# Kernel optimization log

Hardware: AMD Instinct MI355X
Metric: run time of the kernel (lower is better)

Reference implementation:

```python
import jax, jax.numpy as jnp
import numpy as np

EPS = 1e-5  # torch LayerNorm default
H, DH = 8, 64  # heads, dim_head


def _ln(x, g, b):
    mu = jnp.mean(x, axis=-1, keepdims=True)
    var = jnp.var(x, axis=-1, keepdims=True)
    return (x - mu) / jnp.sqrt(var + EPS) * g + b


def setup_inputs() -> dict:
    key = jax.random.key(0)
    ks = jax.random.split(key, 8)
    B, N, M, D, CD = 4, 2048, 256, 1024, 768
    J = M + 1 + N  # context + null + self
    return {
        "x": jax.random.normal(ks[0], (B, N, D), jnp.float32),
        "context": jax.random.normal(ks[1], (B, M, CD), jnp.float32),
        "att_bias": jax.random.normal(ks[2], (B, H, N, J), jnp.float32) * 0.02,
        "ln_g": jnp.ones((D,), jnp.float32),
        "ln_b": jnp.zeros((D,), jnp.float32),
        "null_kv": jax.random.normal(ks[3], (2, DH), jnp.float32),
        "Wq": jax.random.normal(ks[4], (D, H * DH), jnp.float32) * 0.02,
        "Wkv": jax.random.normal(ks[5], (D, 2 * DH), jnp.float32) * 0.02,
        "cln_g": jnp.ones((CD,), jnp.float32),
        "cln_b": jnp.zeros((CD,), jnp.float32),
        "Wc": jax.random.normal(ks[6], (CD, 2 * DH), jnp.float32) * 0.02,
        "bc": jnp.zeros((2 * DH,), jnp.float32),
        "Wo": jax.random.normal(ks[7], (H * DH, D), jnp.float32) * 0.02,
        "oln_g": jnp.ones((D,), jnp.float32),
        "oln_b": jnp.zeros((D,), jnp.float32),
    }


def reference(x, context, att_bias, ln_g, ln_b, null_kv, Wq, Wkv,
              cln_g, cln_b, Wc, bc, Wo, oln_g, oln_b):
    B, N, D = x.shape
    scale = DH ** -0.5
    xn = _ln(x, ln_g, ln_b)
    # queries: per-head [b,h,n,dh], pre-scaled
    q = (xn @ Wq).reshape(B, N, H, DH).transpose(0, 2, 1, 3) * scale
    # shared single-head k/v [b,n,dh]
    kv = xn @ Wkv
    k, v = kv[..., :DH], kv[..., DH:]
    # context k/v [b,m,dh]
    ckv = _ln(context, cln_g, cln_b) @ Wc + bc
    ck, cv = ckv[..., :DH], ckv[..., DH:]
    # null kv token [b,1,dh]
    nk = jnp.broadcast_to(null_kv[0], (B, 1, DH))
    nv = jnp.broadcast_to(null_kv[1], (B, 1, DH))
    # torch order: cat null first, then context -> (ck, nk, k)
    k = jnp.concatenate([ck, nk, k], axis=1)  # [b, j, dh]
    v = jnp.concatenate([cv, nv, v], axis=1)
    score = jnp.einsum('bhid,bjd->bhij', q, k) + att_bias
    probs = jax.nn.softmax(score.astype(jnp.float32), axis=-1).astype(v.dtype)
    att = jnp.einsum('bhij,bjd->bhid', probs, v)
    att = att.transpose(0, 2, 1, 3).reshape(B, N, H * DH)
    return _ln(att @ Wo, oln_g, oln_b)
```

## Files before the change

kernel.cpp:

```cpp
#include <hip/hip_runtime.h>
#include <hip/hip_bf16.h>
#include <cstdint>
#include <cstddef>

#define Bq  4
#define Nq  2048
#define Mq  256
#define Dq  1024
#define CDq 768
#define Hq  8
#define DHq 64
#define Jq  2305
#define QKVN 640
#define NCH 37
#define J2  (NCH * 64)

typedef __bf16  bf16x8 __attribute__((ext_vector_type(8)));
typedef float   f32x4  __attribute__((ext_vector_type(4)));
typedef float   f32x4u __attribute__((ext_vector_type(4), aligned(4)));
typedef float   f32x16 __attribute__((ext_vector_type(16)));
typedef short   s16x8  __attribute__((ext_vector_type(8)));
typedef short   s16x4  __attribute__((ext_vector_type(4)));
typedef unsigned int u32x4 __attribute__((ext_vector_type(4)));
typedef unsigned short u16;
typedef unsigned int   u32;

__device__ __forceinline__ u16 f2b(float v) {
  unsigned x = __builtin_bit_cast(unsigned, v);
  unsigned r = (x + 0x7fffu + ((x >> 16) & 1u)) >> 16;
  return (u16)r;
}
__device__ __forceinline__ float b2f(u16 u) {
  unsigned x = ((unsigned)u) << 16;
  return __builtin_bit_cast(float, x);
}
__device__ __forceinline__ u32 cvtpk(float lo, float hi) {
  u32 r;
  asm("v_cvt_pk_bf16_f32 %0, %1, %2" : "=v"(r) : "v"(lo), "v"(hi));
  return r;
}
__device__ __forceinline__ void pswap(u32& a, u32& b) {
  asm volatile("v_permlane32_swap_b32 %0, %1" : "+v"(a), "+v"(b));
}
__device__ __forceinline__ f32x4 mfma16(bf16x8 a, bf16x8 b, f32x4 c) {
  return __builtin_amdgcn_mfma_f32_16x16x32_bf16(a, b, c, 0, 0, 0);
}
__device__ __forceinline__ f32x16 mfma32(bf16x8 a, bf16x8 b, f32x16 c) {
  return __builtin_amdgcn_mfma_f32_32x32x16_bf16(a, b, c, 0, 0, 0);
}
__device__ __forceinline__ bf16x8 frag_ld(const u16* p) {
  return __builtin_bit_cast(bf16x8, *(const s16x8*)p);
}
__device__ __forceinline__ void stout(float* p, float v) { *p = v; }
__device__ __forceinline__ void stout(u16*   p, float v) { *p = f2b(v); }

__device__ __forceinline__ void gl_lds16(const void* gSrc, void* ldsDst) {
  __builtin_amdgcn_global_load_lds(
      (const __attribute__((address_space(1))) void*)gSrc,
      (__attribute__((address_space(3))) void*)ldsDst, 16, 0, 0);
}

__global__ __launch_bounds__(256) void prep_kernel(
    const float* __restrict__ x,   const float* __restrict__ ln_g,
    const float* __restrict__ ln_b, u16* __restrict__ xn,
    const float* __restrict__ ctx, const float* __restrict__ cln_g,
    const float* __restrict__ cln_b, u16* __restrict__ ctxn,
    const float* __restrict__ Wq, const float* __restrict__ Wkv,
    const float* __restrict__ Wc, const float* __restrict__ Wo,
    u16* __restrict__ WqkvT, u16* __restrict__ WcT, u16* __restrict__ WoT) {
  const int tid = threadIdx.x;
  if (blockIdx.x < Bq * Nq + Bq * Mq) {
    const int row = blockIdx.x;
    const float* in; const float* g; const float* bb; u16* out; int D;
    if (row < Bq * Nq) {
      in = x + (size_t)row * Dq; g = ln_g; bb = ln_b;
      out = xn + (size_t)row * Dq; D = Dq;
    } else {
      int r2 = row - Bq * Nq;
      in = ctx + (size_t)r2 * CDq; g = cln_g; bb = cln_b;
      out = ctxn + (size_t)r2 * CDq; D = CDq;
    }
    __shared__ float buf[1024];
    __shared__ float red[8];
    float s = 0.f, s2 = 0.f;
    for (int i = tid; i < D; i += 256) {
      float v = in[i];
      buf[i] = v;
      s += v; s2 += v * v;
    }
    #pragma unroll
    for (int off = 32; off; off >>= 1) {
      s  += __shfl_down(s,  off);
      s2 += __shfl_down(s2, off);
    }
    if ((tid & 63) == 0) { red[tid >> 6] = s; red[4 + (tid >> 6)] = s2; }
    __syncthreads();
    float sum = red[0] + red[1] + red[2] + red[3];
    float sq  = red[4] + red[5] + red[6] + red[7];
    float mean = sum / D;
    float var  = sq / D - mean * mean;
    float rstd = rsqrtf(var + 1e-5f);
    for (int i = tid; i < D; i += 256)
      out[i] = f2b((buf[i] - mean) * rstd * g[i] + bb[i]);
  } else {
    __shared__ float T[32][33];
    int bid = blockIdx.x - (Bq * Nq + Bq * Mq);
    const float* W; u16* WT; int K, N, bx, by;
    if (bid < 512)      { W = Wq;  WT = WqkvT;                    K = 1024; N = 512;  bx = bid % 16;        by = bid / 16; }
    else if (bid < 640) { W = Wkv; WT = WqkvT + (size_t)512*1024; K = 1024; N = 128;  bx = (bid-512) % 4;   by = (bid-512) / 4; }
    else if (bid < 736) { W = Wc;  WT = WcT;                      K = 768;  N = 128;  bx = (bid-640) % 4;   by = (bid-640) / 4; }
    else                { W = Wo;  WT = WoT;                      K = 512;  N = 1024; bx = (bid-736) % 32;  by = (bid-736) / 32; }
    const int n0 = bx * 32, k0 = by * 32;
    const int tx = tid & 31, ty = tid >> 5;
    #pragma unroll
    for (int i = 0; i < 32; i += 8)
      T[ty + i][tx] = W[(size_t)(k0 + ty + i) * N + n0 + tx];
    __syncthreads();
    #pragma unroll
    for (int i = 0; i < 32; i += 8)
      WT[(size_t)(n0 + ty + i) * K + k0 + tx] = f2b(T[tx][ty + i]);
  }
}

__global__ __launch_bounds__(256) void ln_out_kernel(
    const u16* __restrict__ in, const float* __restrict__ g,
    const float* __restrict__ bb, float* __restrict__ out) {
  const int row = blockIdx.x;
  const int tid = threadIdx.x;
  __shared__ float buf[1024];
  __shared__ float red[8];
  const u16* xr = in + (size_t)row * Dq;
  float s = 0.f, s2 = 0.f;
  {
    s16x4 v4 = *(const s16x4*)(xr + tid * 4);
    #pragma unroll
    for (int e = 0; e < 4; ++e) {
      float v = b2f((u16)v4[e]);
      buf[tid * 4 + e] = v;
      s += v; s2 += v * v;
    }
  }
  #pragma unroll
  for (int off = 32; off; off >>= 1) {
    s  += __shfl_down(s,  off);
    s2 += __shfl_down(s2, off);
  }
  if ((tid & 63) == 0) { red[tid >> 6] = s; red[4 + (tid >> 6)] = s2; }
  __syncthreads();
  float sum = red[0] + red[1] + red[2] + red[3];
  float sq  = red[4] + red[5] + red[6] + red[7];
  float mean = sum / Dq;
  float var  = sq / Dq - mean * mean;
  float rstd = rsqrtf(var + 1e-5f);
  #pragma unroll
  for (int e = 0; e < 4; ++e) {
    int i = tid * 4 + e;
    out[(size_t)row * Dq + i] = (buf[i] - mean) * rstd * g[i] + bb[i];
  }
}

template <typename OT>
__device__ __forceinline__ void gemm_body(const u16* __restrict__ A,
                                          const u16* __restrict__ BT,
                                          OT* __restrict__ C,
                                          int N, int K, int m0, int n0,
                                          u16* Al, u16* Bl) {
  const int tid  = threadIdx.x;
  const int lane = tid & 63, wave = tid >> 6;
  const int l16  = lane & 15, lhi = lane >> 4;
  const int wm = (wave >> 1) * 64, wn = (wave & 1) * 64;

  const int offB = (wave << 10) + (lane << 4);
  const int srow = offB >> 6;
  const int scby = offB & 63;

  f32x4 acc[4][4];
  #pragma unroll
  for (int i = 0; i < 4; ++i)
    #pragma unroll
    for (int j = 0; j < 4; ++j) acc[i][j] = f32x4{0.f, 0.f, 0.f, 0.f};

  for (int k0 = 0; k0 < K; k0 += 32) {
    __syncthreads();
    #pragma unroll
    for (int c = 0; c < 2; ++c) {
      gl_lds16((const char*)(A  + (size_t)(m0 + srow + c * 64) * K + k0) + scby,
               (char*)Al + c * 4096 + (wave << 10));
      gl_lds16((const char*)(BT + (size_t)(n0 + srow + c * 64) * K + k0) + scby,
               (char*)Bl + c * 4096 + (wave << 10));
    }
    __syncthreads();

    bf16x8 af[4], bfr[4];
    #pragma unroll
    for (int mt = 0; mt < 4; ++mt)
      af[mt] = frag_ld(Al + (wm + mt * 16 + l16) * 32 + lhi * 8);
    #pragma unroll
    for (int nt = 0; nt < 4; ++nt)
      bfr[nt] = frag_ld(Bl + (wn + nt * 16 + l16) * 32 + lhi * 8);
    __builtin_amdgcn_s_setprio(1);
    #pragma unroll
    for (int mt = 0; mt < 4; ++mt)
      #pragma unroll
      for (int nt = 0; nt < 4; ++nt)
        acc[mt][nt] = mfma16(af[mt], bfr[nt], acc[mt][nt]);
    __builtin_amdgcn_s_setprio(0);
  }

  #pragma unroll
  for (int mt = 0; mt < 4; ++mt)
    #pragma unroll
    for (int nt = 0; nt < 4; ++nt)
      #pragma unroll
      for (int r = 0; r < 4; ++r)
        stout(C + (size_t)(m0 + wm + mt * 16 + lhi * 4 + r) * N
                + (n0 + wn + nt * 16 + l16),
              acc[mt][nt][r]);
}

__global__ __launch_bounds__(256) void gemm_qkv_ckv(
    const u16* __restrict__ xn, const u16* __restrict__ WqkvT,
    u16* __restrict__ qkv,
    const u16* __restrict__ ctxn, const u16* __restrict__ WcT,
    u16* __restrict__ ckvb) {
  const u16 *A, *BT; u16* C; int N, K, m0, n0;
  if (blockIdx.y < 5) {
    A = xn; BT = WqkvT; C = qkv; N = QKVN; K = Dq;
    m0 = blockIdx.x * 128; n0 = blockIdx.y * 128;
  } else {
    if (blockIdx.x >= 8) return;
    A = ctxn; BT = WcT; C = ckvb; N = 2 * DHq; K = CDq;
    m0 = blockIdx.x * 128; n0 = 0;
  }
  __shared__ __align__(16) u16 Al[128 * 32];
  __shared__ __align__(16) u16 Bl[128 * 32];
  gemm_body<u16>(A, BT, C, N, K, m0, n0, Al, Bl);
}

__global__ __launch_bounds__(256) void gemm128b(const u16* __restrict__ A,
                                                const u16* __restrict__ BT,
                                                u16* __restrict__ C,
                                                int N, int K) {
  __shared__ __align__(16) u16 Al[128 * 32];
  __shared__ __align__(16) u16 Bl[128 * 32];
  gemm_body<u16>(A, BT, C, N, K, blockIdx.x * 128, blockIdx.y * 128, Al, Bl);
}

__global__ void build_kv(const u16* __restrict__ qkv,
                         const u16* __restrict__ ckvb,
                         const float* __restrict__ nullkv,
                         const float* __restrict__ bc,
                         u16* __restrict__ Kt, u16* __restrict__ Vt) {
  int idx = blockIdx.x * 256 + threadIdx.x;
  if (idx >= Bq * J2 * 64) return;
  int d = idx & 63;
  int t = idx >> 6;
  int j = t % J2;
  int b = t / J2;
  float k = 0.f, v = 0.f;
  if (j < Mq) {
    const u16* p = ckvb + (size_t)(b * Mq + j) * 128;
    k = b2f(p[d])      + bc[d];
    v = b2f(p[64 + d]) + bc[64 + d];
  } else if (j == Mq) {
    k = nullkv[d];
    v = nullkv[64 + d];
  } else if (j < Jq) {
    const u16* p = qkv + (size_t)(b * Nq + (j - Mq - 1)) * QKVN + 512;
    k = b2f(p[d]);
    v = b2f(p[64 + d]);
  }
  int ch = j >> 6, row = j & 63;
  char* tbase = (char*)Kt + ((size_t)(b * NCH + ch)) * 8192;
  *(u16*)(tbase + row * 128 + ((d << 1) ^ ((row & 7) << 4))) = f2b(k);
  char* vbase = (char*)Vt + ((size_t)(b * NCH + ch)) * 8192;
  *(u16*)(vbase + d * 128 + ((row << 1) ^ ((d & 7) << 4))) = f2b(v);
}

__global__ __launch_bounds__(128) void attn_kernel(
    const u16* __restrict__ qkv, const u16* __restrict__ Kt,
    const u16* __restrict__ Vt, const float* __restrict__ bias,
    u16* __restrict__ att) {
  __shared__ __align__(16) u16 Kl [2][2][4096];
  __shared__ __align__(16) u16 VTl[2][2][4096];
  const int tid  = threadIdx.x;
  const int wave = tid >> 6, lane = tid & 63;
  const int l = lane & 31, hi = lane >> 5;
  const int qt = blockIdx.x, h = blockIdx.y, b = blockIdx.z;
  const int qrow0 = qt * 64 + wave * 32;

  bf16x8 qf[4];
  {
    const u16* qp = qkv + ((size_t)(b * Nq + qrow0 + l)) * QKVN
                        + h * DHq + hi * 8;
    #pragma unroll
    for (int kt = 0; kt < 4; ++kt) qf[kt] = frag_ld(qp + kt * 16);
  }

  float m_s = -INFINITY, l_s = 0.f;
  f32x16 oacc[2];
  #pragma unroll
  for (int dt = 0; dt < 2; ++dt)
    #pragma unroll
    for (int r = 0; r < 16; ++r) oacc[dt][r] = 0.f;

  const float* bp = bias
      + ((size_t)((b * Hq + h) * (size_t)Nq + qrow0 + l)) * Jq + 4 * hi;

  const size_t tb0 = (size_t)b * NCH;
  const int soff = lane << 4;

  auto stage = [&](int buf, int ch) {
    const char* kt_ = (const char*)Kt + (tb0 + ch) * 8192 + soff;
    const char* vt_ = (const char*)Vt + (tb0 + ch) * 8192 + soff;
    char* kl = (char*)&Kl[wave][buf][0];
    char* vl = (char*)&VTl[wave][buf][0];
    #pragma unroll
    for (int i = 0; i < 8; ++i) {
      gl_lds16(kt_ + i * 1024, kl + i * 1024);
      gl_lds16(vt_ + i * 1024, vl + i * 1024);
    }
  };

  auto loadBias = [&](f32x4 (&bv)[2][4], int ch) {
    const int jc = ch * 64;
    if (ch < NCH - 1) {
      #pragma unroll
      for (int jt = 0; jt < 2; ++jt)
        #pragma unroll
        for (int g = 0; g < 4; ++g)
          bv[jt][g] = (f32x4)(*(const f32x4u*)(bp + jc + jt * 32 + 8 * g));
    } else {
      #pragma unroll
      for (int jt = 0; jt < 2; ++jt)
        #pragma unroll
        for (int g = 0; g < 4; ++g)
          #pragma unroll
          for (int e = 0; e < 4; ++e) {
            int jg = jc + jt * 32 + 8 * g + 4 * hi + e;
            bv[jt][g][e] = (jg < Jq) ? bp[jc + jt * 32 + 8 * g + e] : -1e30f;
          }
    }
  };

  f32x4 bvA[2][4], bvB[2][4];
  stage(0, 0);
  loadBias(bvA, 0);

  auto body = [&](int ch, f32x4 (&bvC)[2][4], f32x4 (&bvN)[2][4]) {
    const int cur = ch & 1;
    if (ch + 1 < NCH) {
      stage(cur ^ 1, ch + 1);
      loadBias(bvN, ch + 1);
      asm volatile("s_waitcnt vmcnt(24)" ::: "memory");
    } else {
      asm volatile("s_waitcnt vmcnt(0)" ::: "memory");
    }
    __builtin_amdgcn_sched_barrier(0);

    const char* kbase = (const char*)&Kl[wave][cur][0];
    const char* vbase = (const char*)&VTl[wave][cur][0];

    f32x16 sacc[2];
    #pragma unroll
    for (int jt = 0; jt < 2; ++jt)
      #pragma unroll
      for (int r = 0; r < 16; ++r) sacc[jt][r] = 0.f;
    __builtin_amdgcn_s_setprio(1);
    #pragma unroll
    for (int jt = 0; jt < 2; ++jt) {
      const int row = jt * 32 + l;
      const int sw = (row & 7) << 4;
      #pragma unroll
      for (int kt = 0; kt < 4; ++kt) {
        bf16x8 kf = frag_ld((const u16*)(kbase + row * 128
                                         + ((kt * 32 + hi * 16) ^ sw)));
        sacc[jt] = mfma32(kf, qf[kt], sacc[jt]);
      }
    }
    __builtin_amdgcn_s_setprio(0);

    float sv[2][16];
    #pragma unroll
    for (int jt = 0; jt < 2; ++jt)
      #pragma unroll
      for (int r = 0; r < 16; ++r)
        sv[jt][r] = sacc[jt][r] * 0.125f + bvC[jt][r >> 2][r & 3];

    float pmax = sv[0][0];
    #pragma unroll
    for (int jt = 0; jt < 2; ++jt)
      #pragma unroll
      for (int r = 0; r < 16; ++r) pmax = fmaxf(pmax, sv[jt][r]);
    pmax = fmaxf(pmax, __shfl_xor(pmax, 32));

    if (__any(pmax > m_s + 8.f)) {
      float mnew = fmaxf(m_s, pmax);
      float corr = __expf(m_s - mnew);
      l_s *= corr;
      m_s = mnew;
      #pragma unroll
      for (int r = 0; r < 16; ++r) {
        float c = __shfl(corr, (r & 3) + 8 * (r >> 2) + 4 * hi);
        oacc[0][r] *= c;
        oacc[1][r] *= c;
      }
    }

    float ps = 0.f;
    #pragma unroll
    for (int jt = 0; jt < 2; ++jt)
      #pragma unroll
      for (int r = 0; r < 16; ++r) {
        float pv = __expf(sv[jt][r] - m_s);
        sv[jt][r] = pv;
        ps += pv;
      }
    ps += __shfl_xor(ps, 32);
    l_s += ps;

    u32 pk[2][8];
    #pragma unroll
    for (int jt = 0; jt < 2; ++jt)
      #pragma unroll
      for (int g = 0; g < 4; ++g) {
        pk[jt][2 * g]     = cvtpk(sv[jt][4 * g],     sv[jt][4 * g + 1]);
        pk[jt][2 * g + 1] = cvtpk(sv[jt][4 * g + 2], sv[jt][4 * g + 3]);
      }

    #pragma unroll
    for (int kt = 0; kt < 4; ++kt) {
      const int t = kt & 1, js = kt >> 1;
      u32 a0 = pk[js][4 * t],     b0 = pk[js][4 * t + 2];
      u32 a1 = pk[js][4 * t + 1], b1 = pk[js][4 * t + 3];
      pswap(a0, b0);
      pswap(a1, b1);
      bf16x8 paf = __builtin_bit_cast(bf16x8, u32x4{a0, a1, b0, b1});
      __builtin_amdgcn_s_setprio(1);
      #pragma unroll
      for (int dt = 0; dt < 2; ++dt) {
        const int vrow = dt * 32 + l;
        bf16x8 vf = frag_ld((const u16*)(vbase + vrow * 128
                     + ((kt * 32 + hi * 16) ^ ((vrow & 7) << 4))));
        oacc[dt] = mfma32(paf, vf, oacc[dt]);
      }
      __builtin_amdgcn_s_setprio(0);
    }
  };

  int ch = 0;
  while (true) {
    body(ch, bvA, bvB);
    if (++ch == NCH) break;
    body(ch, bvB, bvA);
    if (++ch == NCH) break;
  }

  float linv = 1.0f / l_s;
  #pragma unroll
  for (int r = 0; r < 16; ++r) {
    const int qo = (r & 3) + 8 * (r >> 2) + 4 * hi;
    float inv = __shfl(linv, qo);
    u16* op = att + ((size_t)(b * Nq + qrow0 + qo)) * (Hq * DHq) + h * DHq + l;
    op[0]  = f2b(oacc[0][r] * inv);
    op[32] = f2b(oacc[1][r] * inv);
  }
}

extern "C" void kernel_launch(void* const* d_in, const int* in_sizes, int n_in,
                              void* d_out, int out_size, void* d_ws, size_t ws_size,
                              hipStream_t stream) {
  const float* x       = (const float*)d_in[0];
  const float* context = (const float*)d_in[1];
  const float* att_bias= (const float*)d_in[2];
  const float* ln_g    = (const float*)d_in[3];
  const float* ln_b    = (const float*)d_in[4];
  const float* null_kv = (const float*)d_in[5];
  const float* Wq      = (const float*)d_in[6];
  const float* Wkv     = (const float*)d_in[7];
  const float* cln_g   = (const float*)d_in[8];
  const float* cln_b   = (const float*)d_in[9];
  const float* Wc      = (const float*)d_in[10];
  const float* bc      = (const float*)d_in[11];
  const float* Wo      = (const float*)d_in[12];
  const float* oln_g   = (const float*)d_in[13];
  const float* oln_b   = (const float*)d_in[14];
  float* out = (float*)d_out;

  char* p = (char*)d_ws;
  auto alloc = [&](size_t bytes) {
    void* r = (void*)p;
    p += (bytes + 255) & ~(size_t)255;
    return r;
  };
  u16* xn     = (u16*)alloc((size_t)Bq * Nq * Dq * 2);
  u16* ctxn   = (u16*)alloc((size_t)Bq * Mq * CDq * 2);
  u16* WqkvT  = (u16*)alloc((size_t)QKVN * Dq * 2);
  u16* WcT    = (u16*)alloc((size_t)2 * DHq * CDq * 2);
  u16* WoT    = (u16*)alloc((size_t)Dq * Hq * DHq * 2);
  u16* qkv    = (u16*)alloc((size_t)Bq * Nq * QKVN * 2);
  u16* ckvb   = (u16*)alloc((size_t)Bq * Mq * 2 * DHq * 2);
  u16* Ktil   = (u16*)alloc((size_t)Bq * NCH * 8192);
  u16* Vtil   = (u16*)alloc((size_t)Bq * NCH * 8192);
  u16* attb   = (u16*)alloc((size_t)Bq * Nq * Hq * DHq * 2);
  u16* y      = (u16*)alloc((size_t)Bq * Nq * Dq * 2);

  prep_kernel<<<Bq * Nq + Bq * Mq + 1248, 256, 0, stream>>>(
      x, ln_g, ln_b, xn, context, cln_g, cln_b, ctxn,
      Wq, Wkv, Wc, Wo, WqkvT, WcT, WoT);

  gemm_qkv_ckv<<<dim3(Bq * Nq / 128, 6), 256, 0, stream>>>(
      xn, WqkvT, qkv, ctxn, WcT, ckvb);

  build_kv<<<(Bq * J2 * 64 + 255) / 256, 256, 0, stream>>>(
      qkv, ckvb, null_kv, bc, Ktil, Vtil);

  attn_kernel<<<dim3(Nq / 64, Hq, Bq), 128, 0, stream>>>(
      qkv, Ktil, Vtil, att_bias, attb);

  gemm128b<<<dim3(Bq * Nq / 128, Dq / 128), 256, 0, stream>>>(
      attb, WoT, y, Dq, Hq * DHq);
  ln_out_kernel<<<Bq * Nq, 256, 0, stream>>>(y, oln_g, oln_b, out);
}
```

Measured before the change: 290.2 us.

## Share staged K/V tiles across all heads in one attention workgroup

The attention kernel now launches one 512-thread workgroup per 32 query rows, with each of the 8 waves handling a different head. Because K and V are single-head and shared by all heads, the waves stage one K/V chunk into LDS together, each wave loading a slice. The per-wave private buffers and manual vmcnt waits are replaced by block-wide __syncthreads, which cuts redundant K/V global-to-LDS traffic. In exchange it adds a full-block barrier every chunk, so the bias prefetch overlap is reduced and waves are tied together in lockstep.

```diff
diff --git a/kernel.cpp b/kernel.cpp
--- a/kernel.cpp
+++ b/kernel.cpp
@@ -277,17 +277,18 @@
   *(u16*)(vbase + d * 128 + ((row << 1) ^ ((d & 7) << 4))) = f2b(v);
 }
 
-__global__ __launch_bounds__(128) void attn_kernel(
+__global__ __launch_bounds__(512) void attn_kernel(
     const u16* __restrict__ qkv, const u16* __restrict__ Kt,
     const u16* __restrict__ Vt, const float* __restrict__ bias,
     u16* __restrict__ att) {
-  __shared__ __align__(16) u16 Kl [2][2][4096];
-  __shared__ __align__(16) u16 VTl[2][2][4096];
+  __shared__ __align__(16) u16 Kl [2][4096];
+  __shared__ __align__(16) u16 VTl[2][4096];
   const int tid  = threadIdx.x;
   const int wave = tid >> 6, lane = tid & 63;
   const int l = lane & 31, hi = lane >> 5;
-  const int qt = blockIdx.x, h = blockIdx.y, b = blockIdx.z;
-  const int qrow0 = qt * 64 + wave * 32;
+  const int qt = blockIdx.x, b = blockIdx.z;
+  const int h = wave;
+  const int qrow0 = qt * 32;
 
   bf16x8 qf[4];
   {
@@ -308,18 +309,13 @@
       + ((size_t)((b * Hq + h) * (size_t)Nq + qrow0 + l)) * Jq + 4 * hi;
 
   const size_t tb0 = (size_t)b * NCH;
-  const int soff = lane << 4;
+  const int soff = (wave << 10) + (lane << 4);
 
   auto stage = [&](int buf, int ch) {
     const char* kt_ = (const char*)Kt + (tb0 + ch) * 8192 + soff;
     const char* vt_ = (const char*)Vt + (tb0 + ch) * 8192 + soff;
-    char* kl = (char*)&Kl[wave][buf][0];
-    char* vl = (char*)&VTl[wave][buf][0];
-    #pragma unroll
-    for (int i = 0; i < 8; ++i) {
-      gl_lds16(kt_ + i * 1024, kl + i * 1024);
-      gl_lds16(vt_ + i * 1024, vl + i * 1024);
-    }
+    gl_lds16(kt_, (char*)&Kl[buf][0]  + (wave << 10));
+    gl_lds16(vt_, (char*)&VTl[buf][0] + (wave << 10));
   };
 
   auto loadBias = [&](f32x4 (&bv)[2][4], int ch) {
@@ -346,20 +342,16 @@
   f32x4 bvA[2][4], bvB[2][4];
   stage(0, 0);
   loadBias(bvA, 0);
+  __syncthreads();
 
   auto body = [&](int ch, f32x4 (&bvC)[2][4], f32x4 (&bvN)[2][4]) {
     const int cur = ch & 1;
     if (ch + 1 < NCH) {
       stage(cur ^ 1, ch + 1);
       loadBias(bvN, ch + 1);
-      asm volatile("s_waitcnt vmcnt(24)" ::: "memory");
-    } else {
-      asm volatile("s_waitcnt vmcnt(0)" ::: "memory");
-    }
-    __builtin_amdgcn_sched_barrier(0);
-
-    const char* kbase = (const char*)&Kl[wave][cur][0];
-    const char* vbase = (const char*)&VTl[wave][cur][0];
+    }
+    const char* kbase = (const char*)&Kl[cur][0];
+    const char* vbase = (const char*)&VTl[cur][0];
 
     f32x16 sacc[2];
     #pragma unroll
@@ -380,18 +372,17 @@
     }
     __builtin_amdgcn_s_setprio(0);
 
-    float sv[2][16];
     #pragma unroll
     for (int jt = 0; jt < 2; ++jt)
       #pragma unroll
       for (int r = 0; r < 16; ++r)
-        sv[jt][r] = sacc[jt][r] * 0.125f + bvC[jt][r >> 2][r & 3];
-
-    float pmax = sv[0][0];
+        sacc[jt][r] = sacc[jt][r] * 0.125f + bvC[jt][r >> 2][r & 3];
+
+    float pmax = sacc[0][0];
     #pragma unroll
     for (int jt = 0; jt < 2; ++jt)
       #pragma unroll
-      for (int r = 0; r < 16; ++r) pmax = fmaxf(pmax, sv[jt][r]);
+      for (int r = 0; r < 16; ++r) pmax = fmaxf(pmax, sacc[jt][r]);
     pmax = fmaxf(pmax, __shfl_xor(pmax, 32));
 
     if (__any(pmax > m_s + 8.f)) {
@@ -412,8 +403,8 @@
     for (int jt = 0; jt < 2; ++jt)
       #pragma unroll
       for (int r = 0; r < 16; ++r) {
-        float pv = __expf(sv[jt][r] - m_s);
-        sv[jt][r] = pv;
+        float pv = __expf(sacc[jt][r] - m_s);
+        sacc[jt][r] = pv;
         ps += pv;
       }
     ps += __shfl_xor(ps, 32);
@@ -424,8 +415,8 @@
     for (int jt = 0; jt < 2; ++jt)
       #pragma unroll
       for (int g = 0; g < 4; ++g) {
-        pk[jt][2 * g]     = cvtpk(sv[jt][4 * g],     sv[jt][4 * g + 1]);
-        pk[jt][2 * g + 1] = cvtpk(sv[jt][4 * g + 2], sv[jt][4 * g + 3]);
+        pk[jt][2 * g]     = cvtpk(sacc[jt][4 * g],     sacc[jt][4 * g + 1]);
+        pk[jt][2 * g + 1] = cvtpk(sacc[jt][4 * g + 2], sacc[jt][4 * g + 3]);
       }
 
     #pragma unroll
@@ -446,6 +437,7 @@
       }
       __builtin_amdgcn_s_setprio(0);
     }
+    __syncthreads();
   };
 
   int ch = 0;
@@ -515,7 +507,7 @@
   build_kv<<<(Bq * J2 * 64 + 255) / 256, 256, 0, stream>>>(
       qkv, ckvb, null_kv, bc, Ktil, Vtil);
 
-  attn_kernel<<<dim3(Nq / 64, Hq, Bq), 128, 0, stream>>>(
+  attn_kernel<<<dim3(Nq / 32, 1, Bq), 512, 0, stream>>>(
       qkv, Ktil, Vtil, att_bias, attb);
 
   gemm128b<<<dim3(Bq * Nq / 128, Dq / 128), 256, 0, stream>>>(
```

New measurement: 249.6 us. 1.16x faster.
